# Performance work log

Hardware: AMD Instinct MI355X
Metric: run time of the kernel (lower is better)

The kernel has to match this reference:

```python
import jax, jax.numpy as jnp
import numpy as np

GH, GW = 8, 8  # hypernetwork patch grid
EPS = 1e-5


def image_coords(b, h, w, dtype):
    # matches get_image_coordinates: channel0 = x (varies along W), channel1 = y (varies along H)
    xs = jnp.linspace(-1.0, 1.0, w, dtype=dtype)
    ys = jnp.linspace(-1.0, 1.0, h, dtype=dtype)
    X = jnp.broadcast_to(xs[None, :], (h, w))
    Y = jnp.broadcast_to(ys[:, None], (h, w))
    g = jnp.stack([X, Y], axis=0)  # [2,H,W]
    return jnp.broadcast_to(g[None], (b, 2, h, w))


def im2col3(x):
    # reflect-pad 3x3 im2col -> [B,C,9,H,W]
    H, W = x.shape[2], x.shape[3]
    xp = jnp.pad(x, ((0, 0), (0, 0), (1, 1), (1, 1)), mode='reflect')
    cols = [xp[:, :, i:i + H, j:j + W] for i in range(3) for j in range(3)]
    return jnp.stack(cols, axis=2)


def meta_dw3(x, wsig):
    # depthwise 3x3 conv with per-patch weights. wsig: [B, C*9, GH, GW]
    B, C, H, W = x.shape
    p, q = H // GH, W // GW
    cols = im2col3(x).reshape(B, C, 9, GH, p, GW, q)
    Wd = wsig.reshape(B, C, 9, GH, GW)
    out = jnp.einsum('bctuivj,bctuv->bcuivj', cols, Wd)
    return out.reshape(B, C, H, W)


def meta_pw(x, wsig, out_nc):
    # pointwise 1x1 conv with per-patch weights. wsig: [B, out_nc*C, GH, GW]
    B, C, H, W = x.shape
    p, q = H // GH, W // GW
    xr = x.reshape(B, C, GH, p, GW, q)
    Wp = wsig.reshape(B, out_nc, C, GH, GW)
    out = jnp.einsum('bcuivj,bocuv->bouivj', xr, Wp)
    return out.reshape(B, out_nc, H, W)


def batch_norm(x, g, b):
    m = jnp.mean(x, (0, 2, 3), keepdims=True)
    v = jnp.var(x, (0, 2, 3), keepdims=True)
    return (x - m) * jax.lax.rsqrt(v + EPS) * g[None, :, None, None] + b[None, :, None, None]


def relu6(x):
    return jnp.clip(x, 0.0, 6.0)


def hpir(x, wsig, out_nc, g_dw, b_dw, g_pw, b_pw):
    # HyperPatchInvertedResidual, expand_ratio=1, stride=1, in_nc != out_nc -> no residual
    C = x.shape[1]
    n_dw = C * 9
    h = relu6(batch_norm(meta_dw3(x, wsig[:, :n_dw]), g_dw, b_dw))
    h = batch_norm(meta_pw(h, wsig[:, n_dw:n_dw + out_nc * C], out_nc), g_pw, b_pw)
    return h


def resize_bilinear(p, hw):
    B, C = p.shape[0], p.shape[1]
    return jax.image.resize(p, (B, C, hw[0], hw[1]), method='bilinear')


def decoder_forward(x_img, f0, f1, w0, w1, w2,
                    g_dw0, b_dw0, g_pw0, b_pw0,
                    g_dw1, b_dw1, g_pw1, b_pw1,
                    g_dw2, b_dw2, g_pw2, b_pw2):
    feats = [x_img, f0, f1]  # [img] + features[:-1]
    level_w = [w0, w1, w2]
    level_out = [64, 32, 21]
    bn_p = [(g_dw0, b_dw0, g_pw0, b_pw0),
            (g_dw1, b_dw1, g_pw1, b_pw1),
            (g_dw2, b_dw2, g_pw2, b_pw2)]
    p = None
    for level in range(3):
        f = feats[-level - 1]
        if p is None:
            p = f
        else:
            if p.shape[2:] != f.shape[2:]:
                p = resize_bilinear(p, f.shape[2:])
            p = jnp.concatenate([f, p], axis=1)
        B, _, H, W = p.shape
        p = jnp.concatenate([image_coords(B, H, W, p.dtype), p], axis=1)
        g_dw, b_dw, g_pw, b_pw = bn_p[level]
        p = hpir(p, level_w[level], level_out[level], g_dw, b_dw, g_pw, b_pw)
    return p


def setup_inputs() -> dict:
    key = jax.random.key(0)
    ks = jax.random.split(key, 8)
    inp = {
        'x_img': jax.random.normal(ks[0], (4, 3, 256, 256), jnp.float32),
        'f0': jax.random.normal(ks[1], (4, 32, 64, 64), jnp.float32),
        'f1': jax.random.normal(ks[2], (4, 64, 32, 32), jnp.float32),
        'w0': jax.random.normal(ks[3], (4, 4818, 8, 8), jnp.float32) * 0.1,
        'w1': jax.random.normal(ks[4], (4, 4018, 8, 8), jnp.float32) * 0.1,
        'w2': jax.random.normal(ks[5], (4, 1110, 8, 8), jnp.float32) * 0.1,
    }
    for name, c in [('dw0', 66), ('pw0', 64), ('dw1', 98), ('pw1', 32), ('dw2', 37), ('pw2', 21)]:
        inp['g_' + name] = jnp.ones((c,), jnp.float32)
        inp['b_' + name] = jnp.zeros((c,), jnp.float32)
    return inp


def reference(x_img, f0, f1, w0, w1, w2,
              g_dw0, b_dw0, g_pw0, b_pw0,
              g_dw1, b_dw1, g_pw1, b_pw1,
              g_dw2, b_dw2, g_pw2, b_pw2):
    return decoder_forward(x_img, f0, f1, w0, w1, w2,
                           g_dw0, b_dw0, g_pw0, b_pw0,
                           g_dw1, b_dw1, g_pw1, b_pw1,
                           g_dw2, b_dw2, g_pw2, b_pw2)
```

## Files before the change

### kernel.cpp

```cpp
#include <hip/hip_runtime.h>

#define EPS 1e-5f

__device__ __forceinline__ int reflect_idx(int i, int n) {
    if (i < 0) return -i;
    if (i >= n) return 2 * n - 2 - i;
    return i;
}

__device__ __forceinline__ float bilin(const float* __restrict__ pb, int Hp, float sy, float sx) {
    int y0 = (int)floorf(sy), x0 = (int)floorf(sx);
    float fy = sy - y0, fx = sx - x0;
    int y0c = min(max(y0, 0), Hp - 1), y1c = min(max(y0 + 1, 0), Hp - 1);
    int x0c = min(max(x0, 0), Hp - 1), x1c = min(max(x0 + 1, 0), Hp - 1);
    float v00 = pb[y0c * Hp + x0c], v01 = pb[y0c * Hp + x1c];
    float v10 = pb[y1c * Hp + x0c], v11 = pb[y1c * Hp + x1c];
    return v00 * (1 - fy) * (1 - fx) + v01 * (1 - fy) * fx
         + v10 * fy * (1 - fx) + v11 * fy * fx;
}

template <int LEVEL>
__global__ __launch_bounds__(256)
void fused_dw_kernel(const float* __restrict__ feat, const float* __restrict__ prev,
                     const float* __restrict__ pss, const float* __restrict__ wsig,
                     float* __restrict__ out, float* __restrict__ part) {
    constexpr int C    = LEVEL == 0 ? 66 : LEVEL == 1 ? 98 : 37;
    constexpr int H    = LEVEL == 0 ? 32 : LEVEL == 1 ? 64 : 256;
    constexpr int TILE = LEVEL == 2 ? 32 : 16;
    constexpr int NT   = H / TILE;
    constexpr int PXPT = (TILE * TILE) / 256;
    constexpr int WC   = LEVEL == 0 ? 4818 : LEVEL == 1 ? 4018 : 1110;
    constexpr int NF   = LEVEL == 0 ? 64 : LEVEL == 1 ? 32 : 3;
    constexpr int Hp   = LEVEL == 1 ? 32 : 64;
    constexpr int Cp   = LEVEL == 1 ? 64 : 32;
    constexpr int P    = H / 8;
    constexpr float SC = LEVEL == 1 ? 0.5f : 0.25f;
    constexpr int HS   = TILE + 2;

    __shared__ float sh[HS * HS];
    int tid = threadIdx.x, bid = blockIdx.x;
    int tile = bid % (NT * NT);
    int c = (bid / (NT * NT)) % C;
    int b = bid / (NT * NT * C);
    int ty0 = (tile / NT) * TILE, tx0 = (tile % NT) * TILE;

    for (int i = tid; i < HS * HS; i += 256) {
        int h = reflect_idx(ty0 - 1 + i / HS, H);
        int w = reflect_idx(tx0 - 1 + i % HS, H);
        float val;
        if (c == 0)      val = -1.f + 2.f * w / (H - 1);
        else if (c == 1) val = -1.f + 2.f * h / (H - 1);
        else if (c < 2 + NF) val = feat[((size_t)(b * NF + c - 2) * H + h) * H + w];
        else {
            int o = c - 2 - NF;
            const float* pb = prev + (size_t)(b * Cp + o) * Hp * Hp;
            float raw = bilin(pb, Hp, (h + 0.5f) * SC - 0.5f, (w + 0.5f) * SC - 0.5f);
            val = raw * pss[2 * o] + pss[2 * o + 1];
        }
        sh[i] = val;
    }
    __syncthreads();

    float s1 = 0.f, s2 = 0.f;
    float* ob = out + (((size_t)(b * C + c)) * H + ty0) * H + tx0;
    float wreg[9];
    if constexpr (TILE == P) {
        const float* wb = wsig + ((size_t)(b * WC + c * 9)) * 64 + (ty0 / P) * 8 + (tx0 / P);
#pragma unroll
        for (int t = 0; t < 9; ++t) wreg[t] = wb[(size_t)t * 64];
    }
#pragma unroll
    for (int k = 0; k < PXPT; ++k) {
        int px = tid + k * 256;
        int tyy = px / TILE, txx = px % TILE;
        if constexpr (TILE != P) {
            int u = (ty0 + tyy) / P, vv = (tx0 + txx) / P;
            const float* wb = wsig + ((size_t)(b * WC + c * 9)) * 64 + u * 8 + vv;
#pragma unroll
            for (int t = 0; t < 9; ++t) wreg[t] = wb[(size_t)t * 64];
        }
        float acc = 0.f;
#pragma unroll
        for (int t = 0; t < 9; ++t)
            acc += wreg[t] * sh[(tyy + t / 3) * HS + txx + t % 3];
        ob[tyy * H + txx] = acc;
        s1 += acc; s2 += acc * acc;
    }
#pragma unroll
    for (int off = 32; off; off >>= 1) {
        s1 += __shfl_xor(s1, off);
        s2 += __shfl_xor(s2, off);
    }
    __shared__ float r1[4], r2[4];
    int wave = tid >> 6;
    if ((tid & 63) == 0) { r1[wave] = s1; r2[wave] = s2; }
    __syncthreads();
    if (tid == 0) {
        int slot = bid & 63;
        atomicAdd(&part[slot * 2 * C + 2 * c],     r1[0] + r1[1] + r1[2] + r1[3]);
        atomicAdd(&part[slot * 2 * C + 2 * c + 1], r2[0] + r2[1] + r2[2] + r2[3]);
    }
}

__global__ void red_kernel(const float* __restrict__ part, const float* __restrict__ g,
                           const float* __restrict__ bb, float* __restrict__ ss,
                           int C, float invN) {
    int c = threadIdx.x;
    if (c >= C) return;
    float s1 = 0.f, s2 = 0.f;
    for (int s = 0; s < 64; ++s) {
        s1 += part[s * 2 * C + 2 * c];
        s2 += part[s * 2 * C + 2 * c + 1];
    }
    float m = s1 * invN;
    float var = s2 * invN - m * m;
    float sc = g[c] * rsqrtf(var + EPS);
    ss[2 * c] = sc;
    ss[2 * c + 1] = bb[c] - m * sc;
}

template <int C, int ONC, int H, int PX_T, int OC_T>
__global__ __launch_bounds__(256)
void pw_small_kernel(const float* __restrict__ x, const float* __restrict__ wsig,
                     const float* __restrict__ ss, float* __restrict__ out,
                     float* __restrict__ part, int WC, int ndw) {
    constexpr int P = H / 8;
    constexpr int OC_I = ONC / OC_T;
    __shared__ float lw[ONC * C];
    __shared__ float lx[C * PX_T];
    int tid = threadIdx.x, bid = blockIdx.x;
    int uv = bid & 63, b = bid >> 6;
    int u = uv >> 3, v = uv & 7;

    const size_t wbase = ((size_t)b * WC + ndw) * 64 + uv;
    for (int i = tid; i < ONC * C; i += 256) lw[i] = wsig[wbase + (size_t)i * 64];
    for (int i = tid; i < C * PX_T; i += 256) {
        int c = i / PX_T, pxl = i % PX_T;
        int h = u * P + pxl / P, w = v * P + pxl % P;
        float xv = x[(((size_t)b * C + c) * H + h) * H + w];
        lx[i] = fminf(fmaxf(xv * ss[2 * c] + ss[2 * c + 1], 0.f), 6.f);
    }
    __syncthreads();

    int px_id = tid % PX_T, oc_id = tid / PX_T;
    int h = u * P + px_id / P, w = v * P + px_id % P;
    float acc[OC_I];
#pragma unroll
    for (int oi = 0; oi < OC_I; ++oi) acc[oi] = 0.f;
    for (int c = 0; c < C; ++c) {
        float xv = lx[c * PX_T + px_id];
#pragma unroll
        for (int oi = 0; oi < OC_I; ++oi)
            acc[oi] += lw[(oc_id * OC_I + oi) * C + c] * xv;
    }
    float* ob = out + (((size_t)b * ONC) * H + h) * H + w;
#pragma unroll
    for (int oi = 0; oi < OC_I; ++oi)
        ob[(size_t)(oc_id * OC_I + oi) * H * H] = acc[oi];

    constexpr int GROUP = (PX_T < 64) ? PX_T : 64;
    int lane = tid & 63;
    int slot = bid & 63;
#pragma unroll
    for (int oi = 0; oi < OC_I; ++oi) {
        float s1 = acc[oi], s2 = acc[oi] * acc[oi];
#pragma unroll
        for (int off = GROUP / 2; off; off >>= 1) {
            s1 += __shfl_xor(s1, off);
            s2 += __shfl_xor(s2, off);
        }
        if ((lane & (GROUP - 1)) == 0) {
            int o = oc_id * OC_I + oi;
            atomicAdd(&part[slot * 2 * ONC + 2 * o], s1);
            atomicAdd(&part[slot * 2 * ONC + 2 * o + 1], s2);
        }
    }
}

__global__ __launch_bounds__(256)
void pw2_kernel(const float* __restrict__ x, const float* __restrict__ wsig,
                const float* __restrict__ ss, float* __restrict__ out,
                float* __restrict__ part) {
    const int C = 37, ONC = 21, H = 256, PATCH = 32, WC = 1110, NDW = 333;
    __shared__ float lw[ONC * C];
    __shared__ float lsc[C], lsh[C];
    __shared__ float r1[4][ONC], r2[4][ONC];
    int tid = threadIdx.x, bid = blockIdx.x;
    int uv = bid & 63, b = bid >> 6;
    int y0 = (uv >> 3) * PATCH, x0 = (uv & 7) * PATCH;

    for (int i = tid; i < ONC * C; i += 256) lw[i] = wsig[((size_t)(b * WC + NDW) + i) * 64 + uv];
    for (int c = tid; c < C; c += 256) { lsc[c] = ss[2 * c]; lsh[c] = ss[2 * c + 1]; }
    __syncthreads();

    int row = tid >> 3, col = (tid & 7) * 4;
    const float* xb = x + (((size_t)b * C) * H + y0 + row) * H + x0 + col;
    float4 acc[ONC];
#pragma unroll
    for (int o = 0; o < ONC; ++o) acc[o] = make_float4(0.f, 0.f, 0.f, 0.f);

    for (int c = 0; c < C; ++c) {
        float4 xv = *(const float4*)(xb + (size_t)c * H * H);
        float sc = lsc[c], sb = lsh[c];
        xv.x = fminf(fmaxf(xv.x * sc + sb, 0.f), 6.f);
        xv.y = fminf(fmaxf(xv.y * sc + sb, 0.f), 6.f);
        xv.z = fminf(fmaxf(xv.z * sc + sb, 0.f), 6.f);
        xv.w = fminf(fmaxf(xv.w * sc + sb, 0.f), 6.f);
#pragma unroll
        for (int o = 0; o < ONC; ++o) {
            float wv = lw[o * C + c];
            acc[o].x += wv * xv.x;
            acc[o].y += wv * xv.y;
            acc[o].z += wv * xv.z;
            acc[o].w += wv * xv.w;
        }
    }
    float* ob = out + (((size_t)b * ONC) * H + y0 + row) * H + x0 + col;
#pragma unroll
    for (int o = 0; o < ONC; ++o) *(float4*)(ob + (size_t)o * H * H) = acc[o];

    int wave = tid >> 6, lane = tid & 63;
#pragma unroll
    for (int o = 0; o < ONC; ++o) {
        float s1 = acc[o].x + acc[o].y + acc[o].z + acc[o].w;
        float s2 = acc[o].x * acc[o].x + acc[o].y * acc[o].y
                 + acc[o].z * acc[o].z + acc[o].w * acc[o].w;
#pragma unroll
        for (int off = 32; off; off >>= 1) {
            s1 += __shfl_xor(s1, off);
            s2 += __shfl_xor(s2, off);
        }
        if (lane == 0) { r1[wave][o] = s1; r2[wave][o] = s2; }
    }
    __syncthreads();
    int slot = bid & 63;
    for (int o = tid; o < ONC; o += 256) {
        atomicAdd(&part[slot * 2 * ONC + 2 * o],     r1[0][o] + r1[1][o] + r1[2][o] + r1[3][o]);
        atomicAdd(&part[slot * 2 * ONC + 2 * o + 1], r2[0][o] + r2[1][o] + r2[2][o] + r2[3][o]);
    }
}

__global__ void finalbn_kernel(float* __restrict__ out, const float* __restrict__ ss) {
    int idx = blockIdx.x * 256 + threadIdx.x;
    const int total4 = 4 * 21 * 256 * 256 / 4;
    if (idx >= total4) return;
    int c = (idx / (256 * 256 / 4)) % 21;
    float4 v = ((float4*)out)[idx];
    float sc = ss[2 * c], sb = ss[2 * c + 1];
    v.x = v.x * sc + sb; v.y = v.y * sc + sb; v.z = v.z * sc + sb; v.w = v.w * sc + sb;
    ((float4*)out)[idx] = v;
}

extern "C" void kernel_launch(void* const* d_in, const int* in_sizes, int n_in,
                              void* d_out, int out_size, void* d_ws, size_t ws_size,
                              hipStream_t stream) {
    const float* x_img = (const float*)d_in[0];
    const float* f0    = (const float*)d_in[1];
    const float* f1    = (const float*)d_in[2];
    const float* w0    = (const float*)d_in[3];
    const float* w1    = (const float*)d_in[4];
    const float* w2    = (const float*)d_in[5];
    const float* g_dw0 = (const float*)d_in[6],  *b_dw0 = (const float*)d_in[7];
    const float* g_pw0 = (const float*)d_in[8],  *b_pw0 = (const float*)d_in[9];
    const float* g_dw1 = (const float*)d_in[10], *b_dw1 = (const float*)d_in[11];
    const float* g_pw1 = (const float*)d_in[12], *b_pw1 = (const float*)d_in[13];
    const float* g_dw2 = (const float*)d_in[14], *b_dw2 = (const float*)d_in[15];
    const float* g_pw2 = (const float*)d_in[16], *b_pw2 = (const float*)d_in[17];
    float* out = (float*)d_out;
    float* ws = (float*)d_ws;

    float* part_dw0 = ws;
    float* part_pw0 = ws + 8448;
    float* part_dw1 = ws + 16640;
    float* part_pw1 = ws + 29184;
    float* part_dw2 = ws + 33280;
    float* part_pw2 = ws + 38016;
    float* dw0ss = ws + 40704;
    float* pw0ss = ws + 40836;
    float* dw1ss = ws + 40964;
    float* pw1ss = ws + 41160;
    float* dw2ss = ws + 41224;
    float* pw2ss = ws + 41298;
    float* pw0raw = ws + 41344;
    float* pw1raw = pw0raw + 262144;
    float* bigA   = pw1raw + 524288;

    hipMemsetAsync(ws, 0, 40704 * sizeof(float), stream);

    fused_dw_kernel<0><<<4 * 66 * 4, 256, 0, stream>>>(f1, nullptr, nullptr, w0, bigA, part_dw0);
    red_kernel<<<1, 128, 0, stream>>>(part_dw0, g_dw0, b_dw0, dw0ss, 66, 1.f / 4096.f);
    pw_small_kernel<66, 64, 32, 16, 16><<<256, 256, 0, stream>>>(
        bigA, w0, dw0ss, pw0raw, part_pw0, 4818, 594);
    red_kernel<<<1, 128, 0, stream>>>(part_pw0, g_pw0, b_pw0, pw0ss, 64, 1.f / 4096.f);
    fused_dw_kernel<1><<<4 * 98 * 16, 256, 0, stream>>>(f0, pw0raw, pw0ss, w1, bigA, part_dw1);
    red_kernel<<<1, 128, 0, stream>>>(part_dw1, g_dw1, b_dw1, dw1ss, 98, 1.f / 16384.f);
    pw_small_kernel<98, 32, 64, 64, 4><<<256, 256, 0, stream>>>(
        bigA, w1, dw1ss, pw1raw, part_pw1, 4018, 882);
    red_kernel<<<1, 128, 0, stream>>>(part_pw1, g_pw1, b_pw1, pw1ss, 32, 1.f / 16384.f);
    fused_dw_kernel<2><<<4 * 37 * 64, 256, 0, stream>>>(x_img, pw1raw, pw1ss, w2, bigA, part_dw2);
    red_kernel<<<1, 128, 0, stream>>>(part_dw2, g_dw2, b_dw2, dw2ss, 37, 1.f / 262144.f);
    pw2_kernel<<<256, 256, 0, stream>>>(bigA, w2, dw2ss, out, part_pw2);
    red_kernel<<<1, 128, 0, stream>>>(part_pw2, g_pw2, b_pw2, pw2ss, 21, 1.f / 262144.f);
    finalbn_kernel<<<5376, 256, 0, stream>>>(out, pw2ss);
}
```

Measured before the change: 145.7 us.

## Fuse level-2 depthwise recompute into pointwise kernel, skip dw2 output write

The level-2 depthwise kernel now only gathers batch-norm statistics and no longer writes its 37x256x256x4 output. A new fused kernel rebuilds the input tile in shared memory (coords, image, upsampled previous level), recomputes the depthwise conv, applies BN and relu6, then runs the 21-channel pointwise conv. This removes a large intermediate write and read. In exchange, the tile construction and depthwise arithmetic (including bilinear sampling) are done twice, and a roughly 48KB shared-memory tile may limit occupancy.

```diff
diff --git a/kernel.cpp b/kernel.cpp
--- a/kernel.cpp
+++ b/kernel.cpp
@@ -19,7 +19,7 @@
          + v10 * fy * (1 - fx) + v11 * fy * fx;
 }
 
-template <int LEVEL>
+template <int LEVEL, bool WRITE>
 __global__ __launch_bounds__(256)
 void fused_dw_kernel(const float* __restrict__ feat, const float* __restrict__ prev,
                      const float* __restrict__ pss, const float* __restrict__ wsig,
@@ -83,7 +83,7 @@
 #pragma unroll
         for (int t = 0; t < 9; ++t)
             acc += wreg[t] * sh[(tyy + t / 3) * HS + txx + t % 3];
-        ob[tyy * H + txx] = acc;
+        if constexpr (WRITE) ob[tyy * H + txx] = acc;
         s1 += acc; s2 += acc * acc;
     }
 #pragma unroll
@@ -178,53 +178,72 @@
 }
 
 __global__ __launch_bounds__(256)
-void pw2_kernel(const float* __restrict__ x, const float* __restrict__ wsig,
-                const float* __restrict__ ss, float* __restrict__ out,
-                float* __restrict__ part) {
-    const int C = 37, ONC = 21, H = 256, PATCH = 32, WC = 1110, NDW = 333;
-    __shared__ float lw[ONC * C];
-    __shared__ float lsc[C], lsh[C];
-    __shared__ float r1[4][ONC], r2[4][ONC];
+void fused_dwpw2_kernel(const float* __restrict__ ximg, const float* __restrict__ prev,
+                        const float* __restrict__ pss, const float* __restrict__ wsig,
+                        const float* __restrict__ dss, float* __restrict__ out,
+                        float* __restrict__ part) {
+    const int C = 37, ONC = 21, H = 256, Hp = 64, Cp = 32, WC = 1110, NDW = 333;
+    const int HS = 18;
+    __shared__ float sh[C * HS * HS];
+    __shared__ float ldw[333];
+    __shared__ float lw[777];
+    __shared__ float sdw[74];
+
     int tid = threadIdx.x, bid = blockIdx.x;
-    int uv = bid & 63, b = bid >> 6;
-    int y0 = (uv >> 3) * PATCH, x0 = (uv & 7) * PATCH;
-
-    for (int i = tid; i < ONC * C; i += 256) lw[i] = wsig[((size_t)(b * WC + NDW) + i) * 64 + uv];
-    for (int c = tid; c < C; c += 256) { lsc[c] = ss[2 * c]; lsh[c] = ss[2 * c + 1]; }
-    __syncthreads();
-
-    int row = tid >> 3, col = (tid & 7) * 4;
-    const float* xb = x + (((size_t)b * C) * H + y0 + row) * H + x0 + col;
-    float4 acc[ONC];
-#pragma unroll
-    for (int o = 0; o < ONC; ++o) acc[o] = make_float4(0.f, 0.f, 0.f, 0.f);
+    int tile = bid & 3;
+    int uv = (bid >> 2) & 63;
+    int b = bid >> 8;
+    int y0 = (uv >> 3) * 32 + (tile >> 1) * 16;
+    int x0 = (uv & 7) * 32 + (tile & 1) * 16;
+
+    for (int i = tid; i < 333; i += 256) ldw[i] = wsig[((size_t)b * WC + i) * 64 + uv];
+    for (int i = tid; i < 777; i += 256) lw[i]  = wsig[((size_t)b * WC + NDW + i) * 64 + uv];
+    for (int i = tid; i < 74; i += 256)  sdw[i] = dss[i];
+
+    for (int i = tid; i < C * HS * HS; i += 256) {
+        int c = i / (HS * HS), rem = i % (HS * HS);
+        int h = reflect_idx(y0 - 1 + rem / HS, H);
+        int w = reflect_idx(x0 - 1 + rem % HS, H);
+        float val;
+        if (c == 0)      val = -1.f + 2.f * w / (H - 1);
+        else if (c == 1) val = -1.f + 2.f * h / (H - 1);
+        else if (c < 5)  val = ximg[((size_t)(b * 3 + c - 2) * H + h) * H + w];
+        else {
+            int o = c - 5;
+            const float* pb = prev + (size_t)(b * Cp + o) * Hp * Hp;
+            float raw = bilin(pb, Hp, (h + 0.5f) * 0.25f - 0.5f, (w + 0.5f) * 0.25f - 0.5f);
+            val = raw * pss[2 * o] + pss[2 * o + 1];
+        }
+        sh[i] = val;
+    }
+    __syncthreads();
+
+    int tyy = tid >> 4, txx = tid & 15;
+    float acc[21];
+#pragma unroll
+    for (int o = 0; o < 21; ++o) acc[o] = 0.f;
 
     for (int c = 0; c < C; ++c) {
-        float4 xv = *(const float4*)(xb + (size_t)c * H * H);
-        float sc = lsc[c], sb = lsh[c];
-        xv.x = fminf(fmaxf(xv.x * sc + sb, 0.f), 6.f);
-        xv.y = fminf(fmaxf(xv.y * sc + sb, 0.f), 6.f);
-        xv.z = fminf(fmaxf(xv.z * sc + sb, 0.f), 6.f);
-        xv.w = fminf(fmaxf(xv.w * sc + sb, 0.f), 6.f);
-#pragma unroll
-        for (int o = 0; o < ONC; ++o) {
-            float wv = lw[o * C + c];
-            acc[o].x += wv * xv.x;
-            acc[o].y += wv * xv.y;
-            acc[o].z += wv * xv.z;
-            acc[o].w += wv * xv.w;
-        }
-    }
-    float* ob = out + (((size_t)b * ONC) * H + y0 + row) * H + x0 + col;
-#pragma unroll
-    for (int o = 0; o < ONC; ++o) *(float4*)(ob + (size_t)o * H * H) = acc[o];
-
+        const float* sc = sh + c * (HS * HS) + tyy * HS + txx;
+        float dwv = 0.f;
+#pragma unroll
+        for (int t = 0; t < 9; ++t)
+            dwv += ldw[c * 9 + t] * sc[(t / 3) * HS + t % 3];
+        float xv = fminf(fmaxf(dwv * sdw[2 * c] + sdw[2 * c + 1], 0.f), 6.f);
+#pragma unroll
+        for (int o = 0; o < 21; ++o)
+            acc[o] += lw[o * C + c] * xv;
+    }
+
+    float* ob = out + (((size_t)b * ONC) * H + y0 + tyy) * H + x0 + txx;
+#pragma unroll
+    for (int o = 0; o < 21; ++o) ob[(size_t)o * H * H] = acc[o];
+
+    __shared__ float r1[4][21], r2[4][21];
     int wave = tid >> 6, lane = tid & 63;
 #pragma unroll
-    for (int o = 0; o < ONC; ++o) {
-        float s1 = acc[o].x + acc[o].y + acc[o].z + acc[o].w;
-        float s2 = acc[o].x * acc[o].x + acc[o].y * acc[o].y
-                 + acc[o].z * acc[o].z + acc[o].w * acc[o].w;
+    for (int o = 0; o < 21; ++o) {
+        float s1 = acc[o], s2 = acc[o] * acc[o];
 #pragma unroll
         for (int off = 32; off; off >>= 1) {
             s1 += __shfl_xor(s1, off);
@@ -234,9 +253,9 @@
     }
     __syncthreads();
     int slot = bid & 63;
-    for (int o = tid; o < ONC; o += 256) {
-        atomicAdd(&part[slot * 2 * ONC + 2 * o],     r1[0][o] + r1[1][o] + r1[2][o] + r1[3][o]);
-        atomicAdd(&part[slot * 2 * ONC + 2 * o + 1], r2[0][o] + r2[1][o] + r2[2][o] + r2[3][o]);
+    for (int o = tid; o < 21; o += 256) {
+        atomicAdd(&part[slot * 42 + 2 * o],     r1[0][o] + r1[1][o] + r1[2][o] + r1[3][o]);
+        atomicAdd(&part[slot * 42 + 2 * o + 1], r2[0][o] + r2[1][o] + r2[2][o] + r2[3][o]);
     }
 }
 
@@ -287,19 +306,19 @@
 
     hipMemsetAsync(ws, 0, 40704 * sizeof(float), stream);
 
-    fused_dw_kernel<0><<<4 * 66 * 4, 256, 0, stream>>>(f1, nullptr, nullptr, w0, bigA, part_dw0);
+    fused_dw_kernel<0, true><<<4 * 66 * 4, 256, 0, stream>>>(f1, nullptr, nullptr, w0, bigA, part_dw0);
     red_kernel<<<1, 128, 0, stream>>>(part_dw0, g_dw0, b_dw0, dw0ss, 66, 1.f / 4096.f);
     pw_small_kernel<66, 64, 32, 16, 16><<<256, 256, 0, stream>>>(
         bigA, w0, dw0ss, pw0raw, part_pw0, 4818, 594);
     red_kernel<<<1, 128, 0, stream>>>(part_pw0, g_pw0, b_pw0, pw0ss, 64, 1.f / 4096.f);
-    fused_dw_kernel<1><<<4 * 98 * 16, 256, 0, stream>>>(f0, pw0raw, pw0ss, w1, bigA, part_dw1);
+    fused_dw_kernel<1, true><<<4 * 98 * 16, 256, 0, stream>>>(f0, pw0raw, pw0ss, w1, bigA, part_dw1);
     red_kernel<<<1, 128, 0, stream>>>(part_dw1, g_dw1, b_dw1, dw1ss, 98, 1.f / 16384.f);
     pw_small_kernel<98, 32, 64, 64, 4><<<256, 256, 0, stream>>>(
         bigA, w1, dw1ss, pw1raw, part_pw1, 4018, 882);
     red_kernel<<<1, 128, 0, stream>>>(part_pw1, g_pw1, b_pw1, pw1ss, 32, 1.f / 16384.f);
-    fused_dw_kernel<2><<<4 * 37 * 64, 256, 0, stream>>>(x_img, pw1raw, pw1ss, w2, bigA, part_dw2);
+    fused_dw_kernel<2, false><<<4 * 37 * 64, 256, 0, stream>>>(x_img, pw1raw, pw1ss, w2, nullptr, part_dw2);
     red_kernel<<<1, 128, 0, stream>>>(part_dw2, g_dw2, b_dw2, dw2ss, 37, 1.f / 262144.f);
-    pw2_kernel<<<256, 256, 0, stream>>>(bigA, w2, dw2ss, out, part_pw2);
+    fused_dwpw2_kernel<<<1024, 256, 0, stream>>>(x_img, pw1raw, pw1ss, w2, dw2ss, out, part_pw2);
     red_kernel<<<1, 128, 0, stream>>>(part_pw2, g_pw2, b_pw2, pw2ss, 21, 1.f / 262144.f);
     finalbn_kernel<<<5376, 256, 0, stream>>>(out, pw2ss);
 }
```

Result: slower. 201.9 us (+38.6%).

## Fold BN stat reduction kernels into consumer kernels and drop red_kernel launches

Applied to the files above, without the earlier changes.

Removes the six single-block red_kernel launches by having each consuming kernel (pw_small, fused_dw levels 1-2, pw2, finalbn) reduce the 64-slot partial sums into shared-memory scale/shift itself. This eliminates launch gaps and serial tiny kernels between stages, at the cost of every block redundantly reading 64*2*C partials at its start. The final BN kernel also becomes a grid-stride loop over 1024 blocks. A WRITE template flag is added but is always true.

```diff
diff --git a/kernel.cpp b/kernel.cpp
--- a/kernel.cpp
+++ b/kernel.cpp
@@ -19,10 +19,31 @@
          + v10 * fy * (1 - fx) + v11 * fy * fx;
 }
 
-template <int LEVEL>
+__device__ __forceinline__ void reduce_ss_lds(const float* __restrict__ part,
+                                              const float* __restrict__ g,
+                                              const float* __restrict__ bb,
+                                              float* ss, int C, float invN, int tid) {
+    for (int c = tid; c < C; c += 256) {
+        float s1 = 0.f, s2 = 0.f;
+#pragma unroll 8
+        for (int s = 0; s < 64; ++s) {
+            s1 += part[s * 2 * C + 2 * c];
+            s2 += part[s * 2 * C + 2 * c + 1];
+        }
+        float m = s1 * invN;
+        float var = s2 * invN - m * m;
+        float sc = g[c] * rsqrtf(var + EPS);
+        ss[2 * c] = sc;
+        ss[2 * c + 1] = bb[c] - m * sc;
+    }
+}
+
+template <int LEVEL, bool WRITE>
 __global__ __launch_bounds__(256)
 void fused_dw_kernel(const float* __restrict__ feat, const float* __restrict__ prev,
-                     const float* __restrict__ pss, const float* __restrict__ wsig,
+                     const float* __restrict__ part_prev, const float* __restrict__ g_prev,
+                     const float* __restrict__ b_prev, float invN_prev,
+                     const float* __restrict__ wsig,
                      float* __restrict__ out, float* __restrict__ part) {
     constexpr int C    = LEVEL == 0 ? 66 : LEVEL == 1 ? 98 : 37;
     constexpr int H    = LEVEL == 0 ? 32 : LEVEL == 1 ? 64 : 256;
@@ -36,13 +57,20 @@
     constexpr int P    = H / 8;
     constexpr float SC = LEVEL == 1 ? 0.5f : 0.25f;
     constexpr int HS   = TILE + 2;
+    constexpr int PSS  = (LEVEL == 0) ? 2 : 2 * Cp;
 
     __shared__ float sh[HS * HS];
+    __shared__ float pssl[PSS];
     int tid = threadIdx.x, bid = blockIdx.x;
     int tile = bid % (NT * NT);
     int c = (bid / (NT * NT)) % C;
     int b = bid / (NT * NT * C);
     int ty0 = (tile / NT) * TILE, tx0 = (tile % NT) * TILE;
+
+    if constexpr (LEVEL != 0) {
+        reduce_ss_lds(part_prev, g_prev, b_prev, pssl, Cp, invN_prev, tid);
+        __syncthreads();
+    }
 
     for (int i = tid; i < HS * HS; i += 256) {
         int h = reflect_idx(ty0 - 1 + i / HS, H);
@@ -55,7 +83,7 @@
             int o = c - 2 - NF;
             const float* pb = prev + (size_t)(b * Cp + o) * Hp * Hp;
             float raw = bilin(pb, Hp, (h + 0.5f) * SC - 0.5f, (w + 0.5f) * SC - 0.5f);
-            val = raw * pss[2 * o] + pss[2 * o + 1];
+            val = raw * pssl[2 * o] + pssl[2 * o + 1];
         }
         sh[i] = val;
     }
@@ -83,7 +111,7 @@
 #pragma unroll
         for (int t = 0; t < 9; ++t)
             acc += wreg[t] * sh[(tyy + t / 3) * HS + txx + t % 3];
-        ob[tyy * H + txx] = acc;
+        if constexpr (WRITE) ob[tyy * H + txx] = acc;
         s1 += acc; s2 += acc * acc;
     }
 #pragma unroll
@@ -102,43 +130,31 @@
     }
 }
 
-__global__ void red_kernel(const float* __restrict__ part, const float* __restrict__ g,
-                           const float* __restrict__ bb, float* __restrict__ ss,
-                           int C, float invN) {
-    int c = threadIdx.x;
-    if (c >= C) return;
-    float s1 = 0.f, s2 = 0.f;
-    for (int s = 0; s < 64; ++s) {
-        s1 += part[s * 2 * C + 2 * c];
-        s2 += part[s * 2 * C + 2 * c + 1];
-    }
-    float m = s1 * invN;
-    float var = s2 * invN - m * m;
-    float sc = g[c] * rsqrtf(var + EPS);
-    ss[2 * c] = sc;
-    ss[2 * c + 1] = bb[c] - m * sc;
-}
-
 template <int C, int ONC, int H, int PX_T, int OC_T>
 __global__ __launch_bounds__(256)
 void pw_small_kernel(const float* __restrict__ x, const float* __restrict__ wsig,
-                     const float* __restrict__ ss, float* __restrict__ out,
-                     float* __restrict__ part, int WC, int ndw) {
+                     const float* __restrict__ part_in, const float* __restrict__ g,
+                     const float* __restrict__ bb, float invN,
+                     float* __restrict__ out, float* __restrict__ part, int WC, int ndw) {
     constexpr int P = H / 8;
     constexpr int OC_I = ONC / OC_T;
     __shared__ float lw[ONC * C];
     __shared__ float lx[C * PX_T];
+    __shared__ float ssl[2 * C];
     int tid = threadIdx.x, bid = blockIdx.x;
     int uv = bid & 63, b = bid >> 6;
     int u = uv >> 3, v = uv & 7;
 
     const size_t wbase = ((size_t)b * WC + ndw) * 64 + uv;
     for (int i = tid; i < ONC * C; i += 256) lw[i] = wsig[wbase + (size_t)i * 64];
+    reduce_ss_lds(part_in, g, bb, ssl, C, invN, tid);
+    __syncthreads();
+
     for (int i = tid; i < C * PX_T; i += 256) {
         int c = i / PX_T, pxl = i % PX_T;
         int h = u * P + pxl / P, w = v * P + pxl % P;
         float xv = x[(((size_t)b * C + c) * H + h) * H + w];
-        lx[i] = fminf(fmaxf(xv * ss[2 * c] + ss[2 * c + 1], 0.f), 6.f);
+        lx[i] = fminf(fmaxf(xv * ssl[2 * c] + ssl[2 * c + 1], 0.f), 6.f);
     }
     __syncthreads();
 
@@ -179,18 +195,19 @@
 
 __global__ __launch_bounds__(256)
 void pw2_kernel(const float* __restrict__ x, const float* __restrict__ wsig,
-                const float* __restrict__ ss, float* __restrict__ out,
-                float* __restrict__ part) {
+                const float* __restrict__ part_in, const float* __restrict__ g,
+                const float* __restrict__ bb,
+                float* __restrict__ out, float* __restrict__ part) {
     const int C = 37, ONC = 21, H = 256, PATCH = 32, WC = 1110, NDW = 333;
     __shared__ float lw[ONC * C];
-    __shared__ float lsc[C], lsh[C];
+    __shared__ float ssl[2 * C];
     __shared__ float r1[4][ONC], r2[4][ONC];
     int tid = threadIdx.x, bid = blockIdx.x;
     int uv = bid & 63, b = bid >> 6;
     int y0 = (uv >> 3) * PATCH, x0 = (uv & 7) * PATCH;
 
     for (int i = tid; i < ONC * C; i += 256) lw[i] = wsig[((size_t)(b * WC + NDW) + i) * 64 + uv];
-    for (int c = tid; c < C; c += 256) { lsc[c] = ss[2 * c]; lsh[c] = ss[2 * c + 1]; }
+    reduce_ss_lds(part_in, g, bb, ssl, C, 1.f / 262144.f, tid);
     __syncthreads();
 
     int row = tid >> 3, col = (tid & 7) * 4;
@@ -201,7 +218,7 @@
 
     for (int c = 0; c < C; ++c) {
         float4 xv = *(const float4*)(xb + (size_t)c * H * H);
-        float sc = lsc[c], sb = lsh[c];
+        float sc = ssl[2 * c], sb = ssl[2 * c + 1];
         xv.x = fminf(fmaxf(xv.x * sc + sb, 0.f), 6.f);
         xv.y = fminf(fmaxf(xv.y * sc + sb, 0.f), 6.f);
         xv.z = fminf(fmaxf(xv.z * sc + sb, 0.f), 6.f);
@@ -235,20 +252,25 @@
     __syncthreads();
     int slot = bid & 63;
     for (int o = tid; o < ONC; o += 256) {
-        atomicAdd(&part[slot * 2 * ONC + 2 * o],     r1[0][o] + r1[1][o] + r1[2][o] + r1[3][o]);
-        atomicAdd(&part[slot * 2 * ONC + 2 * o + 1], r2[0][o] + r2[1][o] + r2[2][o] + r2[3][o]);
-    }
-}
-
-__global__ void finalbn_kernel(float* __restrict__ out, const float* __restrict__ ss) {
-    int idx = blockIdx.x * 256 + threadIdx.x;
+        atomicAdd(&part[slot * 42 + 2 * o],     r1[0][o] + r1[1][o] + r1[2][o] + r1[3][o]);
+        atomicAdd(&part[slot * 42 + 2 * o + 1], r2[0][o] + r2[1][o] + r2[2][o] + r2[3][o]);
+    }
+}
+
+__global__ __launch_bounds__(256)
+void finalbn_kernel(float* __restrict__ out, const float* __restrict__ part_in,
+                    const float* __restrict__ g, const float* __restrict__ bb) {
+    __shared__ float ssl[42];
+    reduce_ss_lds(part_in, g, bb, ssl, 21, 1.f / 262144.f, threadIdx.x);
+    __syncthreads();
     const int total4 = 4 * 21 * 256 * 256 / 4;
-    if (idx >= total4) return;
-    int c = (idx / (256 * 256 / 4)) % 21;
-    float4 v = ((float4*)out)[idx];
-    float sc = ss[2 * c], sb = ss[2 * c + 1];
-    v.x = v.x * sc + sb; v.y = v.y * sc + sb; v.z = v.z * sc + sb; v.w = v.w * sc + sb;
-    ((float4*)out)[idx] = v;
+    for (int idx = blockIdx.x * 256 + threadIdx.x; idx < total4; idx += gridDim.x * 256) {
+        int c = (idx / (256 * 256 / 4)) % 21;
+        float4 v = ((float4*)out)[idx];
+        float sc = ssl[2 * c], sb = ssl[2 * c + 1];
+        v.x = v.x * sc + sb; v.y = v.y * sc + sb; v.z = v.z * sc + sb; v.w = v.w * sc + sb;
+        ((float4*)out)[idx] = v;
+    }
 }
 
 extern "C" void kernel_launch(void* const* d_in, const int* in_sizes, int n_in,
@@ -275,31 +297,22 @@
     float* part_pw1 = ws + 29184;
     float* part_dw2 = ws + 33280;
     float* part_pw2 = ws + 38016;
-    float* dw0ss = ws + 40704;
-    float* pw0ss = ws + 40836;
-    float* dw1ss = ws + 40964;
-    float* pw1ss = ws + 41160;
-    float* dw2ss = ws + 41224;
-    float* pw2ss = ws + 41298;
-    float* pw0raw = ws + 41344;
+    float* pw0raw = ws + 40704;
     float* pw1raw = pw0raw + 262144;
     float* bigA   = pw1raw + 524288;
 
     hipMemsetAsync(ws, 0, 40704 * sizeof(float), stream);
 
-    fused_dw_kernel<0><<<4 * 66 * 4, 256, 0, stream>>>(f1, nullptr, nullptr, w0, bigA, part_dw0);
-    red_kernel<<<1, 128, 0, stream>>>(part_dw0, g_dw0, b_dw0, dw0ss, 66, 1.f / 4096.f);
+    fused_dw_kernel<0, true><<<4 * 66 * 4, 256, 0, stream>>>(
+        f1, nullptr, nullptr, nullptr, nullptr, 0.f, w0, bigA, part_dw0);
     pw_small_kernel<66, 64, 32, 16, 16><<<256, 256, 0, stream>>>(
-        bigA, w0, dw0ss, pw0raw, part_pw0, 4818, 594);
-    red_kernel<<<1, 128, 0, stream>>>(part_pw0, g_pw0, b_pw0, pw0ss, 64, 1.f / 4096.f);
-    fused_dw_kernel<1><<<4 * 98 * 16, 256, 0, stream>>>(f0, pw0raw, pw0ss, w1, bigA, part_dw1);
-    red_kernel<<<1, 128, 0, stream>>>(part_dw1, g_dw1, b_dw1, dw1ss, 98, 1.f / 16384.f);
+        bigA, w0, part_dw0, g_dw0, b_dw0, 1.f / 4096.f, pw0raw, part_pw0, 4818, 594);
+    fused_dw_kernel<1, true><<<4 * 98 * 16, 256, 0, stream>>>(
+        f0, pw0raw, part_pw0, g_pw0, b_pw0, 1.f / 4096.f, w1, bigA, part_dw1);
     pw_small_kernel<98, 32, 64, 64, 4><<<256, 256, 0, stream>>>(
-        bigA, w1, dw1ss, pw1raw, part_pw1, 4018, 882);
-    red_kernel<<<1, 128, 0, stream>>>(part_pw1, g_pw1, b_pw1, pw1ss, 32, 1.f / 16384.f);
-    fused_dw_kernel<2><<<4 * 37 * 64, 256, 0, stream>>>(x_img, pw1raw, pw1ss, w2, bigA, part_dw2);
-    red_kernel<<<1, 128, 0, stream>>>(part_dw2, g_dw2, b_dw2, dw2ss, 37, 1.f / 262144.f);
-    pw2_kernel<<<256, 256, 0, stream>>>(bigA, w2, dw2ss, out, part_pw2);
-    red_kernel<<<1, 128, 0, stream>>>(part_pw2, g_pw2, b_pw2, pw2ss, 21, 1.f / 262144.f);
-    finalbn_kernel<<<5376, 256, 0, stream>>>(out, pw2ss);
-}
+        bigA, w1, part_dw1, g_dw1, b_dw1, 1.f / 16384.f, pw1raw, part_pw1, 4018, 882);
+    fused_dw_kernel<2, true><<<4 * 37 * 64, 256, 0, stream>>>(
+        x_img, pw1raw, part_pw1, g_pw1, b_pw1, 1.f / 16384.f, w2, bigA, part_dw2);
+    pw2_kernel<<<256, 256, 0, stream>>>(bigA, w2, part_dw2, g_dw2, b_dw2, out, part_pw2);
+    finalbn_kernel<<<1024, 256, 0, stream>>>(out, part_pw2, g_pw2, b_pw2);
+}
```

Result: slower. 154.4 us (+6.0%).
